# Kernel tuning notes

Measured on AMD Instinct MI355X. Metric: run time of the kernel, lower is better.

Reference implementation:

```python
import jax, jax.numpy as jnp
import numpy as np

WORD = 30000
NGRAM = 50000
F = WORD + NGRAM
B, L, K = 32, 64, 6
D, H, FFD, NL = 256, 8, 512, 2
EPS = 1e-5


def setup_inputs() -> dict:
    key = jax.random.key(0)
    ks = jax.random.split(key, 16)
    s = 0.02
    return {
        "word_idx": jax.random.randint(ks[0], (B, L), 0, WORD),
        "ngram_idx": jax.random.randint(ks[1], (B, L, K), 0, NGRAM),
        "fc1_w": jax.random.normal(ks[2], (FFD, F), jnp.float32) * s,
        "fc1_b": jax.random.normal(ks[3], (FFD,), jnp.float32) * s,
        "fc2_w": jax.random.normal(ks[4], (D, FFD), jnp.float32) * s,
        "fc2_b": jax.random.normal(ks[5], (D,), jnp.float32) * s,
        "qkv_w": jax.random.normal(ks[6], (NL, 3 * D, D), jnp.float32) * s,
        "qkv_b": jax.random.normal(ks[7], (NL, 3 * D), jnp.float32) * s,
        "out_w": jax.random.normal(ks[8], (NL, D, D), jnp.float32) * s,
        "out_b": jax.random.normal(ks[9], (NL, D), jnp.float32) * s,
        "ln1_g": jnp.ones((NL, D), jnp.float32),
        "ln1_b": jnp.zeros((NL, D), jnp.float32),
        "ff1_w": jax.random.normal(ks[10], (NL, 4 * D, D), jnp.float32) * s,
        "ff1_b": jax.random.normal(ks[11], (NL, 4 * D), jnp.float32) * s,
        "ff2_w": jax.random.normal(ks[12], (NL, D, 4 * D), jnp.float32) * s,
        "ff2_b": jax.random.normal(ks[13], (NL, D), jnp.float32) * s,
        "ln2_g": jnp.ones((NL, D), jnp.float32),
        "ln2_b": jnp.zeros((NL, D), jnp.float32),
    }


def _layer_norm(x, g, b):
    m = jnp.mean(x, axis=-1, keepdims=True)
    v = jnp.var(x, axis=-1, keepdims=True)
    return (x - m) * jax.lax.rsqrt(v + EPS) * g + b


def _sparse_vecs(word_idx, ngram_idx):
    # vectorized replacement of the per-token scatter loop: multi-hot [B,L,F]
    b, l = word_idx.shape
    bi = jnp.arange(b)[:, None]
    li = jnp.arange(l)[None, :]
    sv = jnp.zeros((b, l, F), jnp.float32)
    sv = sv.at[bi, li, word_idx].set(1.0)
    sv = sv.at[bi[:, :, None], li[:, :, None], WORD + ngram_idx].set(1.0)
    return sv


def reference(word_idx, ngram_idx, fc1_w, fc1_b, fc2_w, fc2_b, qkv_w, qkv_b,
              out_w, out_b, ln1_g, ln1_b, ff1_w, ff1_b, ff2_w, ff2_b,
              ln2_g, ln2_b):
    sv = _sparse_vecs(word_idx, ngram_idx)
    x = jax.nn.relu(sv @ fc1_w.T + fc1_b)          # [B,L,FFD]
    x = x @ fc2_w.T + fc2_b                        # [B,L,D]
    b, l, d = x.shape
    hd = d // H
    scale = 1.0 / np.sqrt(hd).astype(np.float32)
    for i in range(NL):  # post-norm TransformerEncoderLayer, eval mode (no dropout)
        qkv = x @ qkv_w[i].T + qkv_b[i]
        q, k, v = jnp.split(qkv, 3, axis=-1)
        q = q.reshape(b, l, H, hd).transpose(0, 2, 1, 3)
        k = k.reshape(b, l, H, hd).transpose(0, 2, 1, 3)
        v = v.reshape(b, l, H, hd).transpose(0, 2, 1, 3)
        attn = jax.nn.softmax(jnp.einsum('bhqd,bhkd->bhqk', q, k) * scale, axis=-1)
        o = jnp.einsum('bhqk,bhkd->bhqd', attn, v).transpose(0, 2, 1, 3).reshape(b, l, d)
        o = o @ out_w[i].T + out_b[i]
        x = _layer_norm(x + o, ln1_g[i], ln1_b[i])
        f = jax.nn.relu(x @ ff1_w[i].T + ff1_b[i]) @ ff2_w[i].T + ff2_b[i]
        x = _layer_norm(x + f, ln2_g[i], ln2_b[i])
    return x
```

## Files before the change

kernel.cpp:

```cpp
#include <hip/hip_runtime.h>
#include <hip/hip_bf16.h>
#include <math.h>

#define WORDC 30000
#define F_TOT 80000
#define NTOK  2048
#define DMODEL 256
#define FFDIM 512
#define NHEAD 8
#define HDIM  32
#define SEQL  64

typedef __attribute__((ext_vector_type(8))) short bf16x8;
typedef __attribute__((ext_vector_type(8))) unsigned short u16x8;
typedef __attribute__((ext_vector_type(4))) float f32x4;

__device__ __forceinline__ unsigned short f32_to_bf16_rne(float x) {
    unsigned int u = __float_as_uint(x);
    unsigned int r = (u + 0x7FFFu + ((u >> 16) & 1u)) >> 16;
    return (unsigned short)r;
}

__device__ __forceinline__ u16x8 cvt8(float4 a, float4 b) {
    u16x8 v;
    v[0] = f32_to_bf16_rne(a.x); v[1] = f32_to_bf16_rne(a.y);
    v[2] = f32_to_bf16_rne(a.z); v[3] = f32_to_bf16_rne(a.w);
    v[4] = f32_to_bf16_rne(b.x); v[5] = f32_to_bf16_rne(b.y);
    v[6] = f32_to_bf16_rne(b.z); v[7] = f32_to_bf16_rne(b.w);
    return v;
}

__global__ __launch_bounds__(256) void mark_feats_par(
    const int* __restrict__ word_idx,
    const int* __restrict__ ngram_idx,
    unsigned int* __restrict__ bm)
{
    int i = blockIdx.x * 256 + threadIdx.x;
    int f;
    if (i < NTOK)                f = word_idx[i];
    else if (i < NTOK * 7)       f = WORDC + ngram_idx[i - NTOK];
    else                         return;
    atomicOr(&bm[f >> 5], 1u << (f & 31));
}

__global__ __launch_bounds__(256) void transpose_cvt(
    const float* __restrict__ fc1_w,
    unsigned short* __restrict__ fc1T,
    const unsigned int* __restrict__ bm,
    const float* __restrict__ s0, const float* __restrict__ s1,
    const float* __restrict__ s2, const float* __restrict__ s3,
    unsigned short* __restrict__ d0, unsigned short* __restrict__ d1,
    unsigned short* __restrict__ d2, unsigned short* __restrict__ d3)
{
    __shared__ float tile[320][17];
    const int bid = blockIdx.x;
    const int tid = threadIdx.x;

    if (bid < 8000) {
        const int f0 = (bid % 250) * 320;
        const int j0 = (bid / 250) * 16;

        #pragma unroll
        for (int it = 0; it < 5; ++it) {
            int idx = it * 256 + tid;
            int jr  = idx / 80;
            int c4  = idx - jr * 80;
            float4 v = *(const float4*)&fc1_w[(long)(j0 + jr) * F_TOT + f0 + c4 * 4];
            tile[c4 * 4 + 0][jr] = v.x;
            tile[c4 * 4 + 1][jr] = v.y;
            tile[c4 * 4 + 2][jr] = v.z;
            tile[c4 * 4 + 3][jr] = v.w;
        }
        __syncthreads();

        for (int f = tid; f < 320; f += 256) {
            int fg = f0 + f;
            if ((bm[fg >> 5] >> (fg & 31)) & 1u) {
                u16x8 lo, hi;
                #pragma unroll
                for (int j = 0; j < 8; ++j) {
                    lo[j] = f32_to_bf16_rne(tile[f][j]);
                    hi[j] = f32_to_bf16_rne(tile[f][j + 8]);
                }
                *(u16x8*)&fc1T[(long)fg * FFDIM + j0]     = lo;
                *(u16x8*)&fc1T[(long)fg * FFDIM + j0 + 8] = hi;
            }
        }
    } else {
        int s = bid - 8000;
        int ten = s / 48, b48 = s % 48;
        const float* src; unsigned short* dst; int n4;
        switch (ten) {
            case 0:  src = s0; dst = d0; n4 = 2 * 768 * 256 / 4;  break;
            case 1:  src = s1; dst = d1; n4 = 2 * 256 * 256 / 4;  break;
            case 2:  src = s2; dst = d2; n4 = 2 * 1024 * 256 / 4; break;
            default: src = s3; dst = d3; n4 = 2 * 256 * 1024 / 4; break;
        }
        for (int i = b48 * 256 + tid; i < n4; i += 48 * 256) {
            float4 v = ((const float4*)src)[i];
            ushort4 o;
            o.x = f32_to_bf16_rne(v.x);
            o.y = f32_to_bf16_rne(v.y);
            o.z = f32_to_bf16_rne(v.z);
            o.w = f32_to_bf16_rne(v.w);
            ((ushort4*)dst)[i] = o;
        }
    }
}

__global__ __launch_bounds__(256) void embed_gather(
    const int* __restrict__ word_idx,
    const int* __restrict__ ngram_idx,
    const unsigned short* __restrict__ fc1_wT,
    const float* __restrict__ fc1_b,
    const float* __restrict__ fc2_w,
    const float* __restrict__ fc2_b,
    float* __restrict__ x)
{
    __shared__ int   feats[8][8];
    __shared__ float wmsk[8][8];
    __shared__ float x1[8][FFDIM];

    const int t0  = blockIdx.x * 8;
    const int tid = threadIdx.x;

    if (tid < 8) {
        int t = t0 + tid;
        feats[tid][0] = word_idx[t];
        wmsk[tid][0]  = 1.f;
        #pragma unroll
        for (int k = 0; k < 6; ++k) {
            int f = WORDC + ngram_idx[t * 6 + k];
            bool dup = false;
            for (int s = 1; s <= k; ++s)
                if (feats[tid][s] == f) dup = true;
            feats[tid][1 + k] = f;
            wmsk[tid][1 + k]  = dup ? 0.f : 1.f;
        }
    }
// ... 2 lines not shown
    const float2 bb = *(const float2*)&fc1_b[tid * 2];
    #pragma unroll
    for (int tt = 0; tt < 8; ++tt) {
        float a0 = bb.x, a1 = bb.y;
        #pragma unroll
        for (int s = 0; s < 7; ++s) {
            unsigned int wrd = *(const unsigned int*)
                &fc1_wT[(long)feats[tt][s] * FFDIM + tid * 2];
            float m = wmsk[tt][s];
            a0 += m * __uint_as_float((wrd & 0xFFFFu) << 16);
            a1 += m * __uint_as_float(wrd & 0xFFFF0000u);
        }
        x1[tt][tid * 2 + 0] = fmaxf(a0, 0.f);
        x1[tt][tid * 2 + 1] = fmaxf(a1, 0.f);
    }
    __syncthreads();

    const int d = tid;
    float acc[8];
    float cb = fc2_b[d];
    #pragma unroll
    for (int tt = 0; tt < 8; ++tt) acc[tt] = cb;
    const float* wrow = fc2_w + d * FFDIM;
    for (int k = 0; k < FFDIM; ++k) {
        float wv = wrow[k];
        #pragma unroll
        for (int tt = 0; tt < 8; ++tt) acc[tt] += wv * x1[tt][k];
    }
    #pragma unroll
    for (int tt = 0; tt < 8; ++tt)
        x[(t0 + tt) * DMODEL + d] = acc[tt];
}

__global__ __launch_bounds__(512) void fused_qkv_attn(
    const float* __restrict__ x,
    const unsigned short* __restrict__ Wq,
    const float* __restrict__ bq,
    float* __restrict__ o)
{
    __shared__ unsigned short sA[64 * 264];
    __shared__ unsigned short sWp[8][48 * 72];
    __shared__ unsigned short sQ[64 * 40];
    __shared__ unsigned short sK[64 * 40];
    __shared__ unsigned short sVt[32 * 72];
    __shared__ unsigned short sP[64 * 72];
    __shared__ float sfmx[2][64];
    __shared__ float sfsm[2][64];

    const int b = blockIdx.x >> 3;
    const int h = blockIdx.x & 7;
    const int tid  = threadIdx.x;
    const int lane = tid & 63;
    const int w    = tid >> 6;
    const int rg   = w & 3;
    const int ch   = w >> 2;
    const int fr   = lane & 15;
    const int ksub = lane >> 4;
    const int row0 = b * SEQL;

    #pragma unroll
    for (int j = 0; j < 4; ++j) {
        int c = j * 512 + tid;
        int row = c >> 5, c8 = c & 31;
        const float* ap = &x[(long)(row0 + row) * DMODEL + c8 * 8];
        float4 a0 = *(const float4*)ap;
        float4 a1 = *(const float4*)(ap + 4);
        *(u16x8*)&sA[row * 264 + c8 * 8] = cvt8(a0, a1);
    }

    int lr6[6], grow6[6];
    const int wcc = (lane & 7) * 8;
    #pragma unroll
    for (int j = 0; j < 6; ++j) {
        int lr = j * 8 + (lane >> 3);
        lr6[j] = lr;
        int c = ch * 48 + lr;
        grow6[j] = (c >> 5) * 256 + h * HDIM + (c & 31);
    }
    u16x8 wc[6], wn[6];
    #pragma unroll
    for (int j = 0; j < 6; ++j)
        wc[j] = *(const u16x8*)&Wq[(long)grow6[j] * DMODEL + wcc];

    __syncthreads();

    f32x4 acc[3] = {};
    for (int t = 0; t < 4; ++t) {
        #pragma unroll
        for (int j = 0; j < 6; ++j)
            *(u16x8*)&sWp[w][lr6[j] * 72 + wcc] = wc[j];
        if (t < 3) {
            int k0 = (t + 1) * 64;
            #pragma unroll
            for (int j = 0; j < 6; ++j)
                wn[j] = *(const u16x8*)&Wq[(long)grow6[j] * DMODEL + k0 + wcc];
        }
        #pragma unroll
        for (int kk = 0; kk < 2; ++kk) {
            bf16x8 af = *(bf16x8*)&sA[(rg * 16 + fr) * 264 + t * 64 + kk * 32 + ksub * 8];
            #pragma unroll
            for (int ni = 0; ni < 3; ++ni) {
                bf16x8 bf = *(bf16x8*)&sWp[w][(ni * 16 + fr) * 72 + kk * 32 + ksub * 8];
                acc[ni] = __builtin_amdgcn_mfma_f32_16x16x32_bf16(af, bf, acc[ni], 0, 0, 0);
            }
        }
        if (t < 3) {
            #pragma unroll
            for (int j = 0; j < 6; ++j) wc[j] = wn[j];
        }
    }

    const float scale = 0.17677669529663687f;
    #pragma unroll
    for (int ni = 0; ni < 3; ++ni) {
        int c = ch * 48 + ni * 16 + fr;
        int part = c >> 5, pc = c & 31;
        float bv = bq[part * 256 + h * HDIM + pc];
        #pragma unroll
        for (int r = 0; r < 4; ++r) {
            int row = rg * 16 + ksub * 4 + r;
            float v = acc[ni][r] + bv;
            if (part == 0)      sQ[row * 40 + pc] = f32_to_bf16_rne(v * scale);
            else if (part == 1) sK[row * 40 + pc] = f32_to_bf16_rne(v);
            else                sVt[pc * 72 + row] = f32_to_bf16_rne(v);
        }
    }
    __syncthreads();

    f32x4 s4[2];
    {
        bf16x8 afq = *(bf16x8*)&sQ[(rg * 16 + fr) * 40 + ksub * 8];
        #pragma unroll
        for (int ni = 0; ni < 2; ++ni) {
            bf16x8 bfk = *(bf16x8*)&sK[(ch * 32 + ni * 16 + fr) * 40 + ksub * 8];
            f32x4 z = {};
            s4[ni] = __builtin_amdgcn_mfma_f32_16x16x32_bf16(afq, bfk, z, 0, 0, 0);
        }
    }

    #pragma unroll
    for (int r = 0; r < 4; ++r) {
// ... 12 lines not shown
        float m = fmaxf(sfmx[0][row], sfmx[1][row]);
        float p0 = __expf(s4[0][r] - m);
        float p1 = __expf(s4[1][r] - m);
        sP[row * 72 + ch * 32 + fr]      = f32_to_bf16_rne(p0);
        sP[row * 72 + ch * 32 + 16 + fr] = f32_to_bf16_rne(p1);
        float s = p0 + p1;
        s += __shfl_xor(s, 1);
        s += __shfl_xor(s, 2);
        s += __shfl_xor(s, 4);
        s += __shfl_xor(s, 8);
        if (fr == 0) sfsm[ch][row] = s;
    }
    __syncthreads();
    #pragma unroll
    for (int r = 0; r < 4; ++r) {
        int row = rg * 16 + ksub * 4 + r;
        minv[r] = 1.f / (sfsm[0][row] + sfsm[1][row]);
    }

    f32x4 o4 = {};
    #pragma unroll
    for (int kc = 0; kc < 2; ++kc) {
        bf16x8 afp = *(bf16x8*)&sP[(rg * 16 + fr) * 72 + kc * 32 + ksub * 8];
        bf16x8 bfv = *(bf16x8*)&sVt[(ch * 16 + fr) * 72 + kc * 32 + ksub * 8];
        o4 = __builtin_amdgcn_mfma_f32_16x16x32_bf16(afp, bfv, o4, 0, 0, 0);
    }
    #pragma unroll
    for (int r = 0; r < 4; ++r) {
        int row = row0 + rg * 16 + ksub * 4 + r;
        o[(long)row * DMODEL + h * HDIM + ch * 16 + fr] = o4[r] * minv[r];
    }
}

__global__ __launch_bounds__(512) void outln_ffn(
    const float* __restrict__ attn_raw,
    const unsigned short* __restrict__ Wo,
    const float* __restrict__ bo,
    const float* __restrict__ g1, const float* __restrict__ b1t,
    const unsigned short* __restrict__ W1,
    const float* __restrict__ b1,
    const unsigned short* __restrict__ W2,
    const float* __restrict__ b2,
    const float* __restrict__ g2, const float* __restrict__ b2t,
    float* __restrict__ x)
{
    __shared__ unsigned short sA[16 * 264];
    __shared__ float xnf[8 * 264];
    __shared__ unsigned short x1s[16 * 1032];
    __shared__ unsigned short sWp[8][32 * 72];
    __shared__ float redS[8][8];
    __shared__ float redQ[8][8];

    const int tid  = threadIdx.x;
    const int lane = tid & 63;
    const int w    = tid >> 6;
    const int fr   = lane & 15;
    const int ksub = lane >> 4;
    const int m0   = blockIdx.x * 8;

    const int lrb = lane >> 3;
    const int wcc = (lane & 7) * 8;

    {
        int row = tid >> 5, c8 = tid & 31;
        if (tid < 256) {
            const float* ap = &attn_raw[(long)(m0 + row) * DMODEL + c8 * 8];
            float4 a0 = *(const float4*)ap;
            float4 a1 = *(const float4*)(ap + 4);
            *(u16x8*)&sA[row * 264 + c8 * 8] = cvt8(a0, a1);
        } else {
            u16x8 z = {};
            *(u16x8*)&sA[row * 264 + c8 * 8] = z;
        }
    }

    u16x8 wc[4], wn[4];
    #pragma unroll
    for (int j = 0; j < 4; ++j)
        wc[j] = *(const u16x8*)&Wo[(long)(w * 32 + j * 8 + lrb) * DMODEL + wcc];

    __syncthreads();

    f32x4 acc[2] = {};
    #pragma unroll
    for (int t = 0; t < 4; ++t) {
        #pragma unroll
        for (int j = 0; j < 4; ++j)
            *(u16x8*)&sWp[w][(j * 8 + lrb) * 72 + wcc] = wc[j];
        if (t < 3) {
            int k0 = (t + 1) * 64;
            #pragma unroll
            for (int j = 0; j < 4; ++j)
                wn[j] = *(const u16x8*)&Wo[(long)(w * 32 + j * 8 + lrb) * DMODEL + k0 + wcc];
        }
        #pragma unroll
        for (int kk = 0; kk < 2; ++kk) {
            bf16x8 af = *(bf16x8*)&sA[fr * 264 + t * 64 + kk * 32 + ksub * 8];
            #pragma unroll
            for (int ni = 0; ni < 2; ++ni) {
                bf16x8 bf = *(bf16x8*)&sWp[w][(ni * 16 + fr) * 72 + kk * 32 + ksub * 8];
                acc[ni] = __builtin_amdgcn_mfma_f32_16x16x32_bf16(af, bf, acc[ni], 0, 0, 0);
            }
        }
        if (t < 3) {
            #pragma unroll
            for (int j = 0; j < 4; ++j) wc[j] = wn[j];
        }
    }

    float vres[2][4];
    #pragma unroll
    for (int ni = 0; ni < 2; ++ni) {
        int col = w * 32 + ni * 16 + fr;
        float bv = bo[col];
        #pragma unroll
        for (int r = 0; r < 4; ++r) {
            int rl = ksub * 4 + r;
            vres[ni][r] = (rl < 8)
                ? acc[ni][r] + bv + x[(long)(m0 + rl) * DMODEL + col]
                : 0.f;
        }
    }

    #pragma unroll
    for (int r = 0; r < 4; ++r) {
        float s  = vres[0][r] + vres[1][r];
        float qq = vres[0][r] * vres[0][r] + vres[1][r] * vres[1][r];
        #pragma unroll
        for (int mask = 1; mask < 16; mask <<= 1) {
            s  += __shfl_xor(s, mask);
            qq += __shfl_xor(qq, mask);
        }
        if (fr == 0 && ksub < 2) {
            redS[w][ksub * 4 + r] = s;
            redQ[w][ksub * 4 + r] = qq;
        }
    }
    #pragma unroll
    for (int j = 0; j < 4; ++j)
        wc[j] = *(const u16x8*)&W1[(long)(w * 32 + j * 8 + lrb) * DMODEL + wcc];

    __syncthreads();

    #pragma unroll
    for (int r = 0; r < 4; ++r) {
        int rl = ksub * 4 + r;
        if (rl < 8) {
            float sum = 0.f, sumq = 0.f;
            #pragma unroll
            for (int ww = 0; ww < 8; ++ww) {
                sum  += redS[ww][rl];
                sumq += redQ[ww][rl];
            }
            float mean = sum * (1.f / 256.f);
            float var  = sumq * (1.f / 256.f) - mean * mean;
            float rstd = rsqrtf(var + 1e-5f);
            #pragma unroll
            for (int ni = 0; ni < 2; ++ni) {
                int col = w * 32 + ni * 16 + fr;
                float v = (vres[ni][r] - mean) * rstd * g1[col] + b1t[col];
                xnf[rl * 264 + col] = v;
                sA[rl * 264 + col] = f32_to_bf16_rne(v);
            }
        }
    }
    __syncthreads();

    f32x4 acc2[2] = {};
    for (int t = 0; t < 32; ++t) {
        #pragma unroll
        for (int j = 0; j < 4; ++j)
            *(u16x8*)&sWp[w][(j * 8 + lrb) * 72 + wcc] = wc[j];
        if (t < 31) {
            int tn = t + 1;
            if (tn < 16) {
                int nc = tn >> 2, kq = tn & 3;
                #pragma unroll
                for (int j = 0; j < 4; ++j)
                    wn[j] = *(const u16x8*)&W1[(long)(nc * 256 + w * 32 + j * 8 + lrb) * DMODEL
                                               + kq * 64 + wcc];
            } else {
                int t2 = tn - 16;
                #pragma unroll
                for (int j = 0; j < 4; ++j)
                    wn[j] = *(const u16x8*)&W2[(long)(w * 32 + j * 8 + lrb) * 1024
                                               + t2 * 64 + wcc];
            }
        }
        #pragma unroll
        for (int kk = 0; kk < 2; ++kk) {
            bf16x8 af;
            if (t < 16)
                af = *(bf16x8*)&sA[fr * 264 + (t & 3) * 64 + kk * 32 + ksub * 8];
            else
                af = *(bf16x8*)&x1s[fr * 1032 + (t - 16) * 64 + kk * 32 + ksub * 8];
            #pragma unroll
            for (int ni = 0; ni < 2; ++ni) {
                bf16x8 bf = *(bf16x8*)&sWp[w][(ni * 16 + fr) * 72 + kk * 32 + ksub * 8];
                acc2[ni] = __builtin_amdgcn_mfma_f32_16x16x32_bf16(af, bf, acc2[ni], 0, 0, 0);
            }
        }
        if (t < 16 && (t & 3) == 3) {
            int nc = t >> 2;
            #pragma unroll
            for (int ni = 0; ni < 2; ++ni) {
                int col = nc * 256 + w * 32 + ni * 16 + fr;
                float bv = b1[col];
                #pragma unroll
                for (int r = 0; r < 4; ++r) {
                    int rl = ksub * 4 + r;
                    x1s[rl * 1032 + col] = (rl < 8)
                        ? f32_to_bf16_rne(fmaxf(acc2[ni][r] + bv, 0.f))
                        : (unsigned short)0;
                }
                acc2[ni] = (f32x4){};
            }
        }
        if (t == 15) __syncthreads();
        if (t < 31) {
            #pragma unroll
            for (int j = 0; j < 4; ++j) wc[j] = wn[j];
        }
    }

    float vres2[2][4];
    #pragma unroll
    for (int ni = 0; ni < 2; ++ni) {
        int col = w * 32 + ni * 16 + fr;
        float bv = b2[col];
        #pragma unroll
        for (int r = 0; r < 4; ++r) {
            int rl = ksub * 4 + r;
            vres2[ni][r] = (rl < 8)
                ? acc2[ni][r] + bv + xnf[rl * 264 + col]
                : 0.f;
        }
    }

    #pragma unroll
    for (int r = 0; r < 4; ++r) {
        float s  = vres2[0][r] + vres2[1][r];
        float qq = vres2[0][r] * vres2[0][r] + vres2[1][r] * vres2[1][r];
        #pragma unroll
        for (int mask = 1; mask < 16; mask <<= 1) {
            s  += __shfl_xor(s, mask);
            qq += __shfl_xor(qq, mask);
        }
        if (fr == 0 && ksub < 2) {
            redS[w][ksub * 4 + r] = s;
            redQ[w][ksub * 4 + r] = qq;
        }
    }
    __syncthreads();

    #pragma unroll
    for (int r = 0; r < 4; ++r) {
        int rl = ksub * 4 + r;
        if (rl < 8) {
            float sum = 0.f, sumq = 0.f;
            #pragma unroll
            for (int ww = 0; ww < 8; ++ww) {
                sum  += redS[ww][rl];
                sumq += redQ[ww][rl];
            }
            float mean = sum * (1.f / 256.f);
            float var  = sumq * (1.f / 256.f) - mean * mean;
            float rstd = rsqrtf(var + 1e-5f);
            #pragma unroll
            for (int ni = 0; ni < 2; ++ni) {
                int col = w * 32 + ni * 16 + fr;
                x[(long)(m0 + rl) * DMODEL + col] =
                    (vres2[ni][r] - mean) * rstd * g2[col] + b2t[col];
            }
        }
    }
}

__global__ __launch_bounds__(256) void embed_kernel(
    const int* __restrict__ word_idx,
    const int* __restrict__ ngram_idx,
    const float* __restrict__ fc1_w,
    const float* __restrict__ fc1_b,
    const float* __restrict__ fc2_w,
    const float* __restrict__ fc2_b,
    float* __restrict__ x)
{
    __shared__ int   feats[8][8];
    __shared__ int   nf[8];
    __shared__ float x1[8][FFDIM];

    const int t0  = blockIdx.x * 8;
    const int tid = threadIdx.x;

    if (tid < 8) {
        int t = t0 + tid;
        int cnt = 0;
        feats[tid][cnt++] = word_idx[t];
        for (int k = 0; k < 6; ++k) {
            int f = WORDC + ngram_idx[t * 6 + k];
            bool dup = false;
            for (int s = 1; s < cnt; ++s)
                if (feats[tid][s] == f) dup = true;
            if (!dup) feats[tid][cnt++] = f;
        }
        nf[tid] = cnt;
    }
    __syncthreads();

// ... 141 lines not shown
        float s = 0.f;
        #pragma unroll
        for (int d = 0; d < HDIM; ++d) s += qreg[d] * Kt[jj][d];
        sc[i] = s;
        mx = fmaxf(mx, s);
    }
    mx = fmaxf(mx, __shfl_xor(mx, 1));
    mx = fmaxf(mx, __shfl_xor(mx, 2));

    float sum = 0.f;
    #pragma unroll
    for (int i = 0; i < 16; ++i) {
        float e = __expf(sc[i] - mx);
        S[q][p * 16 + i] = e;
        sum += e;
    }
    sum += __shfl_xor(sum, 1);
    sum += __shfl_xor(sum, 2);
    const float inv = 1.f / sum;
    __syncthreads();

    float acc[8] = {};
    for (int jj = 0; jj < SEQL; ++jj) {
        float pv = S[q][jj];
        #pragma unroll
        for (int d = 0; d < 8; ++d) acc[d] += pv * Vt[jj][p * 8 + d];
    }
    float* orow = o + (long)(b * SEQL + q) * DMODEL + h * HDIM + p * 8;
    float4 o0, o1;
    o0.x = acc[0] * inv; o0.y = acc[1] * inv; o0.z = acc[2] * inv; o0.w = acc[3] * inv;
    o1.x = acc[4] * inv; o1.y = acc[5] * inv; o1.z = acc[6] * inv; o1.w = acc[7] * inv;
    *(float4*)orow = o0;
    *(float4*)(orow + 4) = o1;
}

__global__ __launch_bounds__(256) void add_ln_kernel(
    const float* __restrict__ xin,
    const float* __restrict__ f,
    const float* __restrict__ g,
    const float* __restrict__ bta,
    float* __restrict__ xout)
{
    const int w = threadIdx.x >> 6;
    const int lane = threadIdx.x & 63;
    const int t = blockIdx.x * 4 + w;

    float4 xv = *(const float4*)&xin[(long)t * DMODEL + lane * 4];
    float4 fv = *(const float4*)&f[(long)t * DMODEL + lane * 4];
    float v0 = xv.x + fv.x, v1 = xv.y + fv.y, v2 = xv.z + fv.z, v3 = xv.w + fv.w;

    float s  = v0 + v1 + v2 + v3;
    float sq = v0 * v0 + v1 * v1 + v2 * v2 + v3 * v3;
    #pragma unroll
    for (int off = 1; off < 64; off <<= 1) {
        s  += __shfl_xor(s, off);
        sq += __shfl_xor(sq, off);
    }
    float mean = s * (1.f / 256.f);
    float var  = sq * (1.f / 256.f) - mean * mean;
    float rs   = rsqrtf(var + 1e-5f);

    float4 gv = *(const float4*)&g[lane * 4];
    float4 bv = *(const float4*)&bta[lane * 4];
    float4 o;
    o.x = (v0 - mean) * rs * gv.x + bv.x;
    o.y = (v1 - mean) * rs * gv.y + bv.y;
    o.z = (v2 - mean) * rs * gv.z + bv.z;
    o.w = (v3 - mean) * rs * gv.w + bv.w;
    *(float4*)&xout[(long)t * DMODEL + lane * 4] = o;
}

extern "C" void kernel_launch(void* const* d_in, const int* in_sizes, int n_in,
                              void* d_out, int out_size, void* d_ws, size_t ws_size,
                              hipStream_t stream) {
    const int*   word_idx  = (const int*)d_in[0];
    const int*   ngram_idx = (const int*)d_in[1];
    const float* fc1_w = (const float*)d_in[2];
    const float* fc1_b = (const float*)d_in[3];
    const float* fc2_w = (const float*)d_in[4];
    const float* fc2_b = (const float*)d_in[5];
    const float* qkv_w = (const float*)d_in[6];
    const float* qkv_b = (const float*)d_in[7];
    const float* out_w = (const float*)d_in[8];
    const float* out_b = (const float*)d_in[9];
    const float* ln1_g = (const float*)d_in[10];
    const float* ln1_b = (const float*)d_in[11];
    const float* ff1_w = (const float*)d_in[12];
    const float* ff1_b = (const float*)d_in[13];
    const float* ff2_w = (const float*)d_in[14];
    const float* ff2_b = (const float*)d_in[15];
    const float* ln2_g = (const float*)d_in[16];
    const float* ln2_b = (const float*)d_in[17];

    float* x = (float*)d_out;

    const size_t BM_OFF   = 0;
    const size_t FC1T_OFF = 10240;
    const size_t FC1T_BYTES = (size_t)F_TOT * FFDIM * 2;
    const size_t QKVT_OFF = FC1T_OFF + FC1T_BYTES;
    const size_t QKVT_BYTES = (size_t)2 * 768 * 256 * 2;
    const size_t OUTT_OFF = QKVT_OFF + QKVT_BYTES;
    const size_t OUTT_BYTES = (size_t)2 * 256 * 256 * 2;
    const size_t FF1T_OFF = OUTT_OFF + OUTT_BYTES;
    const size_t FF1T_BYTES = (size_t)2 * 1024 * 256 * 2;
    const size_t FF2T_OFF = FF1T_OFF + FF1T_BYTES;
    const size_t FF2T_BYTES = (size_t)2 * 256 * 1024 * 2;
    const size_t ATTN_OFF = FF2T_OFF + FF2T_BYTES;
    const size_t ATTN_BYTES = (size_t)NTOK * DMODEL * 4;
    const size_t FAST_BYTES = ATTN_OFF + ATTN_BYTES;

    if (ws_size >= FAST_BYTES) {
        unsigned int*   bm   = (unsigned int*)((char*)d_ws + BM_OFF);
        unsigned short* fc1T = (unsigned short*)((char*)d_ws + FC1T_OFF);
        unsigned short* qkvT = (unsigned short*)((char*)d_ws + QKVT_OFF);
        unsigned short* outT = (unsigned short*)((char*)d_ws + OUTT_OFF);
        unsigned short* ff1T = (unsigned short*)((char*)d_ws + FF1T_OFF);
        unsigned short* ff2T = (unsigned short*)((char*)d_ws + FF2T_OFF);
        float* attn_raw = (float*)((char*)d_ws + ATTN_OFF);

        hipMemsetAsync((void*)bm, 0, 10240, stream);
        mark_feats_par<<<56, 256, 0, stream>>>(word_idx, ngram_idx, bm);
        transpose_cvt<<<8192, 256, 0, stream>>>(
            fc1_w, fc1T, bm, qkv_w, out_w, ff1_w, ff2_w, qkvT, outT, ff1T, ff2T);
        embed_gather<<<NTOK / 8, 256, 0, stream>>>(word_idx, ngram_idx, fc1T,
                                                   fc1_b, fc2_w, fc2_b, x);

        for (int i = 0; i < 2; ++i) {
            fused_qkv_attn<<<32 * NHEAD, 512, 0, stream>>>(
                x, qkvT + (long)i * 768 * 256, qkv_b + i * 768, attn_raw);

            outln_ffn<<<NTOK / 8, 512, 0, stream>>>(
                attn_raw, outT + (long)i * 256 * 256, out_b + i * 256,
                ln1_g + i * 256, ln1_b + i * 256,
                ff1T + (long)i * 1024 * 256, ff1_b + i * 1024,
                ff2T + (long)i * 256 * 1024, ff2_b + i * 256,
                ln2_g + i * 256, ln2_b + i * 256, x);
        }
    } else {
        float* wsf      = (float*)d_ws;
        float* qkvbuf   = wsf;
        float* attn_raw = qkvbuf + 2048 * 768;
        float* obuf     = attn_raw + 2048 * 256;
        float* ffbuf    = obuf + 2048 * 256;

        embed_kernel<<<NTOK / 8, 256, 0, stream>>>(word_idx, ngram_idx, fc1_w,
                                                   fc1_b, fc2_w, fc2_b, x);
        for (int i = 0; i < 2; ++i) {
            gemm_bias<false><<<dim3(768 / 64, NTOK / 64), 256, 0, stream>>>(
                x, qkv_w + (long)i * 768 * 256, qkv_b + i * 768, qkvbuf,
                NTOK, 768, 256);
            attn_kernel<<<32 * NHEAD, 256, 0, stream>>>(qkvbuf, attn_raw);
            gemm_bias<false><<<dim3(256 / 64, NTOK / 64), 256, 0, stream>>>(
                attn_raw, out_w + (long)i * 256 * 256, out_b + i * 256, obuf,
                NTOK, 256, 256);
            add_ln_kernel<<<NTOK / 4, 256, 0, stream>>>(x, obuf, ln1_g + i * 256,
                                                        ln1_b + i * 256, x);
            gemm_bias<true><<<dim3(1024 / 64, NTOK / 64), 256, 0, stream>>>(
                x, ff1_w + (long)i * 1024 * 256, ff1_b + i * 1024, ffbuf,
                NTOK, 1024, 256);
            gemm_bias<false><<<dim3(256 / 64, NTOK / 64), 256, 0, stream>>>(
                ffbuf, ff2_w + (long)i * 256 * 1024, ff2_b + i * 256, obuf,
                NTOK, 256, 1024);
            add_ln_kernel<<<NTOK / 4, 256, 0, stream>>>(x, obuf, ln2_g + i * 256,
                                                        ln2_b + i * 256, x);
        }
    }
}
```

Baseline: 133.7 us.

## Split fused out-proj/FFN kernel into separate tiled bf16 GEMMs plus add-LN

After: 148.3 us. +10.9%, slower.

```diff
diff --git a/kernel.cpp b/kernel.cpp
--- a/kernel.cpp
+++ b/kernel.cpp
@@ -222,19 +222,33 @@
     #pragma unroll
     for (int j = 0; j < 6; ++j)
         wc[j] = *(const u16x8*)&Wq[(long)grow6[j] * DMODEL + wcc];
+    #pragma unroll
+    for (int j = 0; j < 6; ++j)
+        wn[j] = *(const u16x8*)&Wq[(long)grow6[j] * DMODEL + 64 + wcc];
 
     __syncthreads();
 
     f32x4 acc[3] = {};
+    #pragma unroll
     for (int t = 0; t < 4; ++t) {
-        #pragma unroll
-        for (int j = 0; j < 6; ++j)
-            *(u16x8*)&sWp[w][lr6[j] * 72 + wcc] = wc[j];
-        if (t < 3) {
-            int k0 = (t + 1) * 64;
+        if ((t & 1) == 0) {
             #pragma unroll
             for (int j = 0; j < 6; ++j)
-                wn[j] = *(const u16x8*)&Wq[(long)grow6[j] * DMODEL + k0 + wcc];
+                *(u16x8*)&sWp[w][lr6[j] * 72 + wcc] = wc[j];
+            if (t + 2 < 4) {
+                #pragma unroll
+                for (int j = 0; j < 6; ++j)
+                    wc[j] = *(const u16x8*)&Wq[(long)grow6[j] * DMODEL + (t + 2) * 64 + wcc];
+            }
+        } else {
+            #pragma unroll
+            for (int j = 0; j < 6; ++j)
+                *(u16x8*)&sWp[w][lr6[j] * 72 + wcc] = wn[j];
+            if (t + 2 < 4) {
+                #pragma unroll
+                for (int j = 0; j < 6; ++j)
+                    wn[j] = *(const u16x8*)&Wq[(long)grow6[j] * DMODEL + (t + 2) * 64 + wcc];
+            }
         }
         #pragma unroll
         for (int kk = 0; kk < 2; ++kk) {
@@ -244,10 +258,6 @@
                 bf16x8 bf = *(bf16x8*)&sWp[w][(ni * 16 + fr) * 72 + kk * 32 + ksub * 8];
                 acc[ni] = __builtin_amdgcn_mfma_f32_16x16x32_bf16(af, bf, acc[ni], 0, 0, 0);
             }
-        }
-        if (t < 3) {
-            #pragma unroll
-            for (int j = 0; j < 6; ++j) wc[j] = wn[j];
         }
     }
 
@@ -326,21 +336,16 @@
     }
 }
 
-__global__ __launch_bounds__(512) void outln_ffn(
+__global__ __launch_bounds__(512) void outln(
     const float* __restrict__ attn_raw,
     const unsigned short* __restrict__ Wo,
     const float* __restrict__ bo,
     const float* __restrict__ g1, const float* __restrict__ b1t,
-    const unsigned short* __restrict__ W1,
-    const float* __restrict__ b1,
-    const unsigned short* __restrict__ W2,
-    const float* __restrict__ b2,
-    const float* __restrict__ g2, const float* __restrict__ b2t,
-    float* __restrict__ x)
+    const float* __restrict__ x,
+    unsigned short* __restrict__ xnb,
+    float* __restrict__ xnf)
 {
     __shared__ unsigned short sA[16 * 264];
-    __shared__ float xnf[8 * 264];
-    __shared__ unsigned short x1s[16 * 1032];
     __shared__ unsigned short sWp[8][32 * 72];
     __shared__ float redS[8][8];
     __shared__ float redQ[8][8];
@@ -430,10 +435,6 @@
             redQ[w][ksub * 4 + r] = qq;
         }
     }
-    #pragma unroll
-    for (int j = 0; j < 4; ++j)
-        wc[j] = *(const u16x8*)&W1[(long)(w * 32 + j * 8 + lrb) * DMODEL + wcc];
-
     __syncthreads();
 
     #pragma unroll
@@ -453,121 +454,116 @@
             for (int ni = 0; ni < 2; ++ni) {
                 int col = w * 32 + ni * 16 + fr;
                 float v = (vres[ni][r] - mean) * rstd * g1[col] + b1t[col];
-                xnf[rl * 264 + col] = v;
-                sA[rl * 264 + col] = f32_to_bf16_rne(v);
+                long idx = (long)(m0 + rl) * DMODEL + col;
+                xnf[idx] = v;
+                xnb[idx] = f32_to_bf16_rne(v);
             }
         }
     }
-    __syncthreads();
-
-    f32x4 acc2[2] = {};
-    for (int t = 0; t < 32; ++t) {
-        #pragma unroll
-        for (int j = 0; j < 4; ++j)
-            *(u16x8*)&sWp[w][(j * 8 + lrb) * 72 + wcc] = wc[j];
-        if (t < 31) {
-            int tn = t + 1;
-            if (tn < 16) {
-                int nc = tn >> 2, kq = tn & 3;
-                #pragma unroll
-                for (int j = 0; j < 4; ++j)
-                    wn[j] = *(const u16x8*)&W1[(long)(nc * 256 + w * 32 + j * 8 + lrb) * DMODEL
-                                               + kq * 64 + wcc];
-            } else {
-                int t2 = tn - 16;
-                #pragma unroll
-                for (int j = 0; j < 4; ++j)
-                    wn[j] = *(const u16x8*)&W2[(long)(w * 32 + j * 8 + lrb) * 1024
-                                               + t2 * 64 + wcc];
+}
+
+template<bool RELU, bool OUT16>
+__global__ __launch_bounds__(256) void gemm_bf16(
+    const unsigned short* __restrict__ A,
+    const unsigned short* __restrict__ Wb,
+    const float* __restrict__ bias,
+    void* __restrict__ Cout,
+    int M, int N, int K)
+{
+    __shared__ unsigned short sA[64 * 40];
+    __shared__ unsigned short sW[64 * 40];
+
+    const int tid  = threadIdx.x;
+    const int lane = tid & 63;
+    const int w    = tid >> 6;
+    const int wr   = w >> 1;
+    const int wc   = w & 1;
+    const int m0   = blockIdx.y * 64;
+    const int n0   = blockIdx.x * 64;
+
+    const int srow = tid >> 2;
+    const int ssub = tid & 3;
+
+    const int fr   = lane & 15;
+    const int ksub = lane >> 4;
+
+    f32x4 acc[2][2] = {};
+
+    for (int k0 = 0; k0 < K; k0 += 32) {
+        u16x8 av = *(const u16x8*)&A[(long)(m0 + srow) * K + k0 + ssub * 8];
+        u16x8 wv = *(const u16x8*)&Wb[(long)(n0 + srow) * K + k0 + ssub * 8];
+
+        __syncthreads();
+        *(u16x8*)&sA[srow * 40 + ssub * 8] = av;
+        *(u16x8*)&sW[srow * 40 + ssub * 8] = wv;
+        __syncthreads();
+
+        #pragma unroll
+        for (int mi = 0; mi < 2; ++mi) {
+            bf16x8 af = *(bf16x8*)&sA[(wr * 32 + mi * 16 + fr) * 40 + ksub * 8];
+            #pragma unroll
+            for (int ni = 0; ni < 2; ++ni) {
+                bf16x8 bf = *(bf16x8*)&sW[(wc * 32 + ni * 16 + fr) * 40 + ksub * 8];
+                acc[mi][ni] = __builtin_amdgcn_mfma_f32_16x16x32_bf16(
+                    af, bf, acc[mi][ni], 0, 0, 0);
             }
         }
-        #pragma unroll
-        for (int kk = 0; kk < 2; ++kk) {
-            bf16x8 af;
-            if (t < 16)
-                af = *(bf16x8*)&sA[fr * 264 + (t & 3) * 64 + kk * 32 + ksub * 8];
-            else
-                af = *(bf16x8*)&x1s[fr * 1032 + (t - 16) * 64 + kk * 32 + ksub * 8];
-            #pragma unroll
-            for (int ni = 0; ni < 2; ++ni) {
-                bf16x8 bf = *(bf16x8*)&sWp[w][(ni * 16 + fr) * 72 + kk * 32 + ksub * 8];
-                acc2[ni] = __builtin_amdgcn_mfma_f32_16x16x32_bf16(af, bf, acc2[ni], 0, 0, 0);
+    }
+
+    #pragma unroll
+    for (int mi = 0; mi < 2; ++mi) {
+        #pragma unroll
+        for (int ni = 0; ni < 2; ++ni) {
+            int col = n0 + wc * 32 + ni * 16 + fr;
+            float bv = bias[col];
+            #pragma unroll
+            for (int r = 0; r < 4; ++r) {
+                int row = m0 + wr * 32 + mi * 16 + ksub * 4 + r;
+                float v = acc[mi][ni][r] + bv;
+                if (RELU) v = fmaxf(v, 0.f);
+                if (OUT16)
+                    ((unsigned short*)Cout)[(long)row * N + col] = f32_to_bf16_rne(v);
+                else
+                    ((float*)Cout)[(long)row * N + col] = v;
             }
         }
-        if (t < 16 && (t & 3) == 3) {
-            int nc = t >> 2;
-            #pragma unroll
-            for (int ni = 0; ni < 2; ++ni) {
-                int col = nc * 256 + w * 32 + ni * 16 + fr;
-                float bv = b1[col];
-                #pragma unroll
-                for (int r = 0; r < 4; ++r) {
-                    int rl = ksub * 4 + r;
-                    x1s[rl * 1032 + col] = (rl < 8)
-                        ? f32_to_bf16_rne(fmaxf(acc2[ni][r] + bv, 0.f))
-                        : (unsigned short)0;
-                }
-                acc2[ni] = (f32x4){};
-            }
-        }
-        if (t == 15) __syncthreads();
-        if (t < 31) {
-            #pragma unroll
-            for (int j = 0; j < 4; ++j) wc[j] = wn[j];
-        }
-    }
-
-    float vres2[2][4];
-    #pragma unroll
-    for (int ni = 0; ni < 2; ++ni) {
-        int col = w * 32 + ni * 16 + fr;
-        float bv = b2[col];
-        #pragma unroll
-        for (int r = 0; r < 4; ++r) {
-            int rl = ksub * 4 + r;
-            vres2[ni][r] = (rl < 8)
-                ? acc2[ni][r] + bv + xnf[rl * 264 + col]
-                : 0.f;
-        }
-    }
-
-    #pragma unroll
-    for (int r = 0; r < 4; ++r) {
-        float s  = vres2[0][r] + vres2[1][r];
-        float qq = vres2[0][r] * vres2[0][r] + vres2[1][r] * vres2[1][r];
-        #pragma unroll
-        for (int mask = 1; mask < 16; mask <<= 1) {
-            s  += __shfl_xor(s, mask);
-            qq += __shfl_xor(qq, mask);
-        }
-        if (fr == 0 && ksub < 2) {
-            redS[w][ksub * 4 + r] = s;
-            redQ[w][ksub * 4 + r] = qq;
-        }
-    }
-    __syncthreads();
-
-    #pragma unroll
-    for (int r = 0; r < 4; ++r) {
-        int rl = ksub * 4 + r;
-        if (rl < 8) {
-            float sum = 0.f, sumq = 0.f;
-            #pragma unroll
-            for (int ww = 0; ww < 8; ++ww) {
-                sum  += redS[ww][rl];
-                sumq += redQ[ww][rl];
-            }
-            float mean = sum * (1.f / 256.f);
-            float var  = sumq * (1.f / 256.f) - mean * mean;
-            float rstd = rsqrtf(var + 1e-5f);
-            #pragma unroll
-            for (int ni = 0; ni < 2; ++ni) {
-                int col = w * 32 + ni * 16 + fr;
-                x[(long)(m0 + rl) * DMODEL + col] =
-                    (vres2[ni][r] - mean) * rstd * g2[col] + b2t[col];
-            }
-        }
-    }
+    }
+}
+
+__global__ __launch_bounds__(256) void add_ln_kernel(
+    const float* __restrict__ xin,
+    const float* __restrict__ f,
+    const float* __restrict__ g,
+    const float* __restrict__ bta,
+    float* __restrict__ xout)
+{
+    const int w = threadIdx.x >> 6;
+    const int lane = threadIdx.x & 63;
+    const int t = blockIdx.x * 4 + w;
+
+    float4 xv = *(const float4*)&xin[(long)t * DMODEL + lane * 4];
+    float4 fv = *(const float4*)&f[(long)t * DMODEL + lane * 4];
+    float v0 = xv.x + fv.x, v1 = xv.y + fv.y, v2 = xv.z + fv.z, v3 = xv.w + fv.w;
+
+    float s  = v0 + v1 + v2 + v3;
+    float sq = v0 * v0 + v1 * v1 + v2 * v2 + v3 * v3;
+    #pragma unroll
+    for (int off = 1; off < 64; off <<= 1) {
+        s  += __shfl_xor(s, off);
+        sq += __shfl_xor(sq, off);
+    }
+    float mean = s * (1.f / 256.f);
+    float var  = sq * (1.f / 256.f) - mean * mean;
+    float rs   = rsqrtf(var + 1e-5f);
+
+    float4 gv = *(const float4*)&g[lane * 4];
+    float4 bv = *(const float4*)&bta[lane * 4];
+    float4 o;
+    o.x = (v0 - mean) * rs * gv.x + bv.x;
+    o.y = (v1 - mean) * rs * gv.y + bv.y;
+    o.z = (v2 - mean) * rs * gv.z + bv.z;
+    o.w = (v3 - mean) * rs * gv.w + bv.w;
+    *(float4*)&xout[(long)t * DMODEL + lane * 4] = o;
 }
 
 __global__ __launch_bounds__(256) void embed_kernel(
@@ -775,42 +771,6 @@
     o1.x = acc[4] * inv; o1.y = acc[5] * inv; o1.z = acc[6] * inv; o1.w = acc[7] * inv;
     *(float4*)orow = o0;
     *(float4*)(orow + 4) = o1;
-}
-
-__global__ __launch_bounds__(256) void add_ln_kernel(
-    const float* __restrict__ xin,
-    const float* __restrict__ f,
-    const float* __restrict__ g,
-    const float* __restrict__ bta,
-    float* __restrict__ xout)
-{
-    const int w = threadIdx.x >> 6;
-    const int lane = threadIdx.x & 63;
-    const int t = blockIdx.x * 4 + w;
-
-    float4 xv = *(const float4*)&xin[(long)t * DMODEL + lane * 4];
-    float4 fv = *(const float4*)&f[(long)t * DMODEL + lane * 4];
-    float v0 = xv.x + fv.x, v1 = xv.y + fv.y, v2 = xv.z + fv.z, v3 = xv.w + fv.w;
-
-    float s  = v0 + v1 + v2 + v3;
-    float sq = v0 * v0 + v1 * v1 + v2 * v2 + v3 * v3;
-    #pragma unroll
-    for (int off = 1; off < 64; off <<= 1) {
-        s  += __shfl_xor(s, off);
-        sq += __shfl_xor(sq, off);
-    }
-    float mean = s * (1.f / 256.f);
-    float var  = sq * (1.f / 256.f) - mean * mean;
-    float rs   = rsqrtf(var + 1e-5f);
-
-    float4 gv = *(const float4*)&g[lane * 4];
-    float4 bv = *(const float4*)&bta[lane * 4];
-    float4 o;
-    o.x = (v0 - mean) * rs * gv.x + bv.x;
-    o.y = (v1 - mean) * rs * gv.y + bv.y;
-    o.z = (v2 - mean) * rs * gv.z + bv.z;
-    o.w = (v3 - mean) * rs * gv.w + bv.w;
-    *(float4*)&xout[(long)t * DMODEL + lane * 4] = o;
 }
 
 extern "C" void kernel_launch(void* const* d_in, const int* in_sizes, int n_in,
@@ -850,7 +810,15 @@
     const size_t FF2T_BYTES = (size_t)2 * 256 * 1024 * 2;
     const size_t ATTN_OFF = FF2T_OFF + FF2T_BYTES;
     const size_t ATTN_BYTES = (size_t)NTOK * DMODEL * 4;
-    const size_t FAST_BYTES = ATTN_OFF + ATTN_BYTES;
+    const size_t XNB_OFF  = ATTN_OFF + ATTN_BYTES;
+    const size_t XNB_BYTES = (size_t)NTOK * DMODEL * 2;
+    const size_t XNF_OFF  = XNB_OFF + XNB_BYTES;
+    const size_t XNF_BYTES = (size_t)NTOK * DMODEL * 4;
+    const size_t FFB_OFF  = XNF_OFF + XNF_BYTES;
+    const size_t FFB_BYTES = (size_t)NTOK * 1024 * 2;
+    const size_t OBUF_OFF = FFB_OFF + FFB_BYTES;
+    const size_t OBUF_BYTES = (size_t)NTOK * DMODEL * 4;
+    const size_t FAST_BYTES = OBUF_OFF + OBUF_BYTES;
 
     if (ws_size >= FAST_BYTES) {
         unsigned int*   bm   = (unsigned int*)((char*)d_ws + BM_OFF);
@@ -860,6 +828,10 @@
         unsigned short* ff1T = (unsigned short*)((char*)d_ws + FF1T_OFF);
         unsigned short* ff2T = (unsigned short*)((char*)d_ws + FF2T_OFF);
         float* attn_raw = (float*)((char*)d_ws + ATTN_OFF);
+        unsigned short* xnb = (unsigned short*)((char*)d_ws + XNB_OFF);
+        float* xnf = (float*)((char*)d_ws + XNF_OFF);
+        unsigned short* ffb = (unsigned short*)((char*)d_ws + FFB_OFF);
+        float* obuf = (float*)((char*)d_ws + OBUF_OFF);
 
         hipMemsetAsync((void*)bm, 0, 10240, stream);
         mark_feats_par<<<56, 256, 0, stream>>>(word_idx, ngram_idx, bm);
@@ -872,12 +844,20 @@
             fused_qkv_attn<<<32 * NHEAD, 512, 0, stream>>>(
                 x, qkvT + (long)i * 768 * 256, qkv_b + i * 768, attn_raw);
 
-            outln_ffn<<<NTOK / 8, 512, 0, stream>>>(
+            outln<<<NTOK / 8, 512, 0, stream>>>(
                 attn_raw, outT + (long)i * 256 * 256, out_b + i * 256,
-                ln1_g + i * 256, ln1_b + i * 256,
-                ff1T + (long)i * 1024 * 256, ff1_b + i * 1024,
-                ff2T + (long)i * 256 * 1024, ff2_b + i * 256,
-                ln2_g + i * 256, ln2_b + i * 256, x);
+                ln1_g + i * 256, ln1_b + i * 256, x, xnb, xnf);
+
+            gemm_bf16<true, true><<<dim3(1024 / 64, NTOK / 64), 256, 0, stream>>>(
+                xnb, ff1T + (long)i * 1024 * 256, ff1_b + i * 1024, ffb,
+                NTOK, 1024, 256);
+
+            gemm_bf16<false, false><<<dim3(256 / 64, NTOK / 64), 256, 0, stream>>>(
+                ffb, ff2T + (long)i * 256 * 1024, ff2_b + i * 256, obuf,
+                NTOK, 256, 1024);
+
+            add_ln_kernel<<<NTOK / 4, 256, 0, stream>>>(
+                xnf, obuf, ln2_g + i * 256, ln2_b + i * 256, x);
         }
     } else {
         float* wsf      = (float*)d_ws;
```

## Pre-pack transformer weights into MFMA fragment layout and load fragments directly

Applied to the files above, without the earlier changes.

Result: faster. 125.4 us (-6.2%).

```diff
diff --git a/kernel.cpp b/kernel.cpp
--- a/kernel.cpp
+++ b/kernel.cpp
@@ -28,6 +28,11 @@
     v[4] = f32_to_bf16_rne(b.x); v[5] = f32_to_bf16_rne(b.y);
     v[6] = f32_to_bf16_rne(b.z); v[7] = f32_to_bf16_rne(b.w);
     return v;
+}
+
+__device__ __forceinline__ bf16x8 ldfrag(const unsigned short* F, int ntile,
+                                          int KT, int ktile, int lane) {
+    return *(const bf16x8*)&F[(((long)(ntile * KT + ktile) * 64 + lane) << 3)];
 }
 
 __global__ __launch_bounds__(256) void mark_feats_par(
@@ -87,24 +92,24 @@
             }
         }
     } else {
-        int s = bid - 8000;
-        int ten = s / 48, b48 = s % 48;
-        const float* src; unsigned short* dst; int n4;
-        switch (ten) {
-            case 0:  src = s0; dst = d0; n4 = 2 * 768 * 256 / 4;  break;
-            case 1:  src = s1; dst = d1; n4 = 2 * 256 * 256 / 4;  break;
-            case 2:  src = s2; dst = d2; n4 = 2 * 1024 * 256 / 4; break;
-            default: src = s3; dst = d3; n4 = 2 * 256 * 1024 / 4; break;
-        }
-        for (int i = b48 * 256 + tid; i < n4; i += 48 * 256) {
-            float4 v = ((const float4*)src)[i];
-            ushort4 o;
-            o.x = f32_to_bf16_rne(v.x);
-            o.y = f32_to_bf16_rne(v.y);
-            o.z = f32_to_bf16_rne(v.z);
-            o.w = f32_to_bf16_rne(v.w);
-            ((ushort4*)dst)[i] = o;
-        }
+        long fid = (long)(bid - 8000) * 256 + tid;
+        const float* src; unsigned short* dst; int K; long base;
+        if (fid < 49152)        { src = s0; dst = d0; K = 256;  base = fid; }
+        else if (fid < 65536)   { src = s1; dst = d1; K = 256;  base = fid - 49152; }
+        else if (fid < 131072)  { src = s2; dst = d2; K = 256;  base = fid - 65536; }
+        else                    { src = s3; dst = d3; K = 1024; base = fid - 131072; }
+        int lane = (int)(base & 63);
+        long t   = base >> 6;
+        int KT   = K >> 5;
+        int ntile = (int)(t / KT);
+        int ktile = (int)(t - (long)ntile * KT);
+        int row = ntile * 16 + (lane & 15);
+        int k   = ktile * 32 + (lane >> 4) * 8;
+        const float* sp = src + (long)row * K + k;
+        u16x8 v;
+        #pragma unroll
+        for (int j = 0; j < 8; ++j) v[j] = f32_to_bf16_rne(sp[j]);
+        *(u16x8*)&dst[base << 3] = v;
     }
 }
 
@@ -173,14 +178,13 @@
         x[(t0 + tt) * DMODEL + d] = acc[tt];
 }
 
-__global__ __launch_bounds__(512) void fused_qkv_attn(
+__global__ __launch_bounds__(512, 4) void fused_qkv_attn(
     const float* __restrict__ x,
-    const unsigned short* __restrict__ Wq,
+    const unsigned short* __restrict__ WqF,
     const float* __restrict__ bq,
     float* __restrict__ o)
 {
     __shared__ unsigned short sA[64 * 264];
-    __shared__ unsigned short sWp[8][48 * 72];
     __shared__ unsigned short sQ[64 * 40];
     __shared__ unsigned short sK[64 * 40];
     __shared__ unsigned short sVt[32 * 72];
@@ -199,6 +203,14 @@
     const int ksub = lane >> 4;
     const int row0 = b * SEQL;
 
+    int nt[3];
+    #pragma unroll
+    for (int ni = 0; ni < 3; ++ni) {
+        int c = ch * 48 + ni * 16;
+        int part = c >> 5, pcb = c & 31;
+        nt[ni] = (part * 256 + h * HDIM + pcb) >> 4;
+    }
+
     #pragma unroll
     for (int j = 0; j < 4; ++j) {
         int c = j * 512 + tid;
@@ -209,45 +221,37 @@
         *(u16x8*)&sA[row * 264 + c8 * 8] = cvt8(a0, a1);
     }
 
-    int lr6[6], grow6[6];
-    const int wcc = (lane & 7) * 8;
-    #pragma unroll
-    for (int j = 0; j < 6; ++j) {
-        int lr = j * 8 + (lane >> 3);
-        lr6[j] = lr;
-        int c = ch * 48 + lr;
-        grow6[j] = (c >> 5) * 256 + h * HDIM + (c & 31);
-    }
-    u16x8 wc[6], wn[6];
-    #pragma unroll
-    for (int j = 0; j < 6; ++j)
-        wc[j] = *(const u16x8*)&Wq[(long)grow6[j] * DMODEL + wcc];
+    bf16x8 wf[2][2][3];
+    #pragma unroll
+    for (int kk = 0; kk < 2; ++kk)
+        #pragma unroll
+        for (int ni = 0; ni < 3; ++ni)
+            wf[0][kk][ni] = ldfrag(WqF, nt[ni], 8, kk, lane);
+    #pragma unroll
+    for (int kk = 0; kk < 2; ++kk)
+        #pragma unroll
+        for (int ni = 0; ni < 3; ++ni)
+            wf[1][kk][ni] = ldfrag(WqF, nt[ni], 8, 2 + kk, lane);
 
     __syncthreads();
 
     f32x4 acc[3] = {};
+    #pragma unroll
     for (int t = 0; t < 4; ++t) {
-        #pragma unroll
-        for (int j = 0; j < 6; ++j)
-            *(u16x8*)&sWp[w][lr6[j] * 72 + wcc] = wc[j];
-        if (t < 3) {
-            int k0 = (t + 1) * 64;
-            #pragma unroll
-            for (int j = 0; j < 6; ++j)
-                wn[j] = *(const u16x8*)&Wq[(long)grow6[j] * DMODEL + k0 + wcc];
-        }
+        const int cur = t & 1;
         #pragma unroll
         for (int kk = 0; kk < 2; ++kk) {
             bf16x8 af = *(bf16x8*)&sA[(rg * 16 + fr) * 264 + t * 64 + kk * 32 + ksub * 8];
             #pragma unroll
-            for (int ni = 0; ni < 3; ++ni) {
-                bf16x8 bf = *(bf16x8*)&sWp[w][(ni * 16 + fr) * 72 + kk * 32 + ksub * 8];
-                acc[ni] = __builtin_amdgcn_mfma_f32_16x16x32_bf16(af, bf, acc[ni], 0, 0, 0);
-            }
-        }
-        if (t < 3) {
-            #pragma unroll
-            for (int j = 0; j < 6; ++j) wc[j] = wn[j];
+            for (int ni = 0; ni < 3; ++ni)
+                acc[ni] = __builtin_amdgcn_mfma_f32_16x16x32_bf16(af, wf[cur][kk][ni], acc[ni], 0, 0, 0);
+        }
+        if (t + 2 < 4) {
+            #pragma unroll
+            for (int kk = 0; kk < 2; ++kk)
+                #pragma unroll
+                for (int ni = 0; ni < 3; ++ni)
+                    wf[cur][kk][ni] = ldfrag(WqF, nt[ni], 8, (t + 2) * 2 + kk, lane);
         }
     }
 
@@ -326,14 +330,14 @@
     }
 }
 
-__global__ __launch_bounds__(512) void outln_ffn(
+__global__ __launch_bounds__(512, 4) void outln_ffn(
     const float* __restrict__ attn_raw,
-    const unsigned short* __restrict__ Wo,
+    const unsigned short* __restrict__ WoF,
     const float* __restrict__ bo,
     const float* __restrict__ g1, const float* __restrict__ b1t,
-    const unsigned short* __restrict__ W1,
+    const unsigned short* __restrict__ W1F,
     const float* __restrict__ b1,
-    const unsigned short* __restrict__ W2,
+    const unsigned short* __restrict__ W2F,
     const float* __restrict__ b2,
     const float* __restrict__ g2, const float* __restrict__ b2t,
     float* __restrict__ x)
@@ -341,7 +345,6 @@
     __shared__ unsigned short sA[16 * 264];
     __shared__ float xnf[8 * 264];
     __shared__ unsigned short x1s[16 * 1032];
-    __shared__ unsigned short sWp[8][32 * 72];
     __shared__ float redS[8][8];
     __shared__ float redQ[8][8];
 
@@ -351,9 +354,6 @@
     const int fr   = lane & 15;
     const int ksub = lane >> 4;
     const int m0   = blockIdx.x * 8;
-
-    const int lrb = lane >> 3;
-    const int wcc = (lane & 7) * 8;
 
     {
         int row = tid >> 5, c8 = tid & 31;
@@ -368,37 +368,37 @@
         }
     }
 
-    u16x8 wc[4], wn[4];
-    #pragma unroll
-    for (int j = 0; j < 4; ++j)
-        wc[j] = *(const u16x8*)&Wo[(long)(w * 32 + j * 8 + lrb) * DMODEL + wcc];
+    bf16x8 wf[2][2][2];
+    #pragma unroll
+    for (int kk = 0; kk < 2; ++kk)
+        #pragma unroll
+        for (int ni = 0; ni < 2; ++ni)
+            wf[0][kk][ni] = ldfrag(WoF, w * 2 + ni, 8, kk, lane);
+    #pragma unroll
+    for (int kk = 0; kk < 2; ++kk)
+        #pragma unroll
+        for (int ni = 0; ni < 2; ++ni)
+            wf[1][kk][ni] = ldfrag(WoF, w * 2 + ni, 8, 2 + kk, lane);
 
     __syncthreads();
 
     f32x4 acc[2] = {};
     #pragma unroll
     for (int t = 0; t < 4; ++t) {
-        #pragma unroll
-        for (int j = 0; j < 4; ++j)
-            *(u16x8*)&sWp[w][(j * 8 + lrb) * 72 + wcc] = wc[j];
-        if (t < 3) {
-            int k0 = (t + 1) * 64;
-            #pragma unroll
-            for (int j = 0; j < 4; ++j)
-                wn[j] = *(const u16x8*)&Wo[(long)(w * 32 + j * 8 + lrb) * DMODEL + k0 + wcc];
-        }
+        const int cur = t & 1;
         #pragma unroll
         for (int kk = 0; kk < 2; ++kk) {
             bf16x8 af = *(bf16x8*)&sA[fr * 264 + t * 64 + kk * 32 + ksub * 8];
             #pragma unroll
-            for (int ni = 0; ni < 2; ++ni) {
-                bf16x8 bf = *(bf16x8*)&sWp[w][(ni * 16 + fr) * 72 + kk * 32 + ksub * 8];
-                acc[ni] = __builtin_amdgcn_mfma_f32_16x16x32_bf16(af, bf, acc[ni], 0, 0, 0);
-            }
-        }
-        if (t < 3) {
-            #pragma unroll
-            for (int j = 0; j < 4; ++j) wc[j] = wn[j];
+            for (int ni = 0; ni < 2; ++ni)
+                acc[ni] = __builtin_amdgcn_mfma_f32_16x16x32_bf16(af, wf[cur][kk][ni], acc[ni], 0, 0, 0);
+        }
+        if (t + 2 < 4) {
+            #pragma unroll
+            for (int kk = 0; kk < 2; ++kk)
+                #pragma unroll
+                for (int ni = 0; ni < 2; ++ni)
+                    wf[cur][kk][ni] = ldfrag(WoF, w * 2 + ni, 8, (t + 2) * 2 + kk, lane);
         }
     }
 
@@ -416,6 +416,15 @@
         }
     }
 
+    bf16x8 wc[2][2], wn[2][2], wn2[2][2];
+    #pragma unroll
+    for (int kk = 0; kk < 2; ++kk)
+        #pragma unroll
+        for (int ni = 0; ni < 2; ++ni) {
+            wc[kk][ni] = ldfrag(W1F, w * 2 + ni, 8, kk, lane);
+            wn[kk][ni] = ldfrag(W1F, w * 2 + ni, 8, 2 + kk, lane);
+        }
+
     #pragma unroll
     for (int r = 0; r < 4; ++r) {
         float s  = vres[0][r] + vres[1][r];
@@ -430,10 +439,6 @@
             redQ[w][ksub * 4 + r] = qq;
         }
     }
-    #pragma unroll
-    for (int j = 0; j < 4; ++j)
-        wc[j] = *(const u16x8*)&W1[(long)(w * 32 + j * 8 + lrb) * DMODEL + wcc];
-
     __syncthreads();
 
     #pragma unroll
@@ -462,23 +467,22 @@
 
     f32x4 acc2[2] = {};
     for (int t = 0; t < 32; ++t) {
-        #pragma unroll
-        for (int j = 0; j < 4; ++j)
-            *(u16x8*)&sWp[w][(j * 8 + lrb) * 72 + wcc] = wc[j];
-        if (t < 31) {
-            int tn = t + 1;
+        if (t < 30) {
+            int tn = t + 2;
             if (tn < 16) {
                 int nc = tn >> 2, kq = tn & 3;
                 #pragma unroll
-                for (int j = 0; j < 4; ++j)
-                    wn[j] = *(const u16x8*)&W1[(long)(nc * 256 + w * 32 + j * 8 + lrb) * DMODEL
-                                               + kq * 64 + wcc];
+                for (int kk = 0; kk < 2; ++kk)
+                    #pragma unroll
+                    for (int ni = 0; ni < 2; ++ni)
+                        wn2[kk][ni] = ldfrag(W1F, nc * 16 + w * 2 + ni, 8, kq * 2 + kk, lane);
             } else {
                 int t2 = tn - 16;
                 #pragma unroll
-                for (int j = 0; j < 4; ++j)
-                    wn[j] = *(const u16x8*)&W2[(long)(w * 32 + j * 8 + lrb) * 1024
-                                               + t2 * 64 + wcc];
+                for (int kk = 0; kk < 2; ++kk)
+                    #pragma unroll
+                    for (int ni = 0; ni < 2; ++ni)
+                        wn2[kk][ni] = ldfrag(W2F, w * 2 + ni, 32, t2 * 2 + kk, lane);
             }
         }
         #pragma unroll
@@ -489,10 +493,8 @@
             else
                 af = *(bf16x8*)&x1s[fr * 1032 + (t - 16) * 64 + kk * 32 + ksub * 8];
             #pragma unroll
-            for (int ni = 0; ni < 2; ++ni) {
-                bf16x8 bf = *(bf16x8*)&sWp[w][(ni * 16 + fr) * 72 + kk * 32 + ksub * 8];
-                acc2[ni] = __builtin_amdgcn_mfma_f32_16x16x32_bf16(af, bf, acc2[ni], 0, 0, 0);
-            }
+            for (int ni = 0; ni < 2; ++ni)
+                acc2[ni] = __builtin_amdgcn_mfma_f32_16x16x32_bf16(af, wc[kk][ni], acc2[ni], 0, 0, 0);
         }
         if (t < 16 && (t & 3) == 3) {
             int nc = t >> 2;
@@ -511,10 +513,13 @@
             }
         }
         if (t == 15) __syncthreads();
-        if (t < 31) {
-            #pragma unroll
-            for (int j = 0; j < 4; ++j) wc[j] = wn[j];
-        }
+        #pragma unroll
+        for (int kk = 0; kk < 2; ++kk)
+            #pragma unroll
+            for (int ni = 0; ni < 2; ++ni) {
+                wc[kk][ni] = wn[kk][ni];
+                wn[kk][ni] = wn2[kk][ni];
+            }
     }
 
     float vres2[2][4];
@@ -855,28 +860,28 @@
     if (ws_size >= FAST_BYTES) {
         unsigned int*   bm   = (unsigned int*)((char*)d_ws + BM_OFF);
         unsigned short* fc1T = (unsigned short*)((char*)d_ws + FC1T_OFF);
-        unsigned short* qkvT = (unsigned short*)((char*)d_ws + QKVT_OFF);
-        unsigned short* outT = (unsigned short*)((char*)d_ws + OUTT_OFF);
-        unsigned short* ff1T = (unsigned short*)((char*)d_ws + FF1T_OFF);
-        unsigned short* ff2T = (unsigned short*)((char*)d_ws + FF2T_OFF);
+        unsigned short* qkvF = (unsigned short*)((char*)d_ws + QKVT_OFF);
+        unsigned short* outF = (unsigned short*)((char*)d_ws + OUTT_OFF);
+        unsigned short* ff1F = (unsigned short*)((char*)d_ws + FF1T_OFF);
+        unsigned short* ff2F = (unsigned short*)((char*)d_ws + FF2T_OFF);
         float* attn_raw = (float*)((char*)d_ws + ATTN_OFF);
 
         hipMemsetAsync((void*)bm, 0, 10240, stream);
         mark_feats_par<<<56, 256, 0, stream>>>(word_idx, ngram_idx, bm);
-        transpose_cvt<<<8192, 256, 0, stream>>>(
-            fc1_w, fc1T, bm, qkv_w, out_w, ff1_w, ff2_w, qkvT, outT, ff1T, ff2T);
+        transpose_cvt<<<8768, 256, 0, stream>>>(
+            fc1_w, fc1T, bm, qkv_w, out_w, ff1_w, ff2_w, qkvF, outF, ff1F, ff2F);
         embed_gather<<<NTOK / 8, 256, 0, stream>>>(word_idx, ngram_idx, fc1T,
                                                    fc1_b, fc2_w, fc2_b, x);
 
         for (int i = 0; i < 2; ++i) {
             fused_qkv_attn<<<32 * NHEAD, 512, 0, stream>>>(
-                x, qkvT + (long)i * 768 * 256, qkv_b + i * 768, attn_raw);
+                x, qkvF + (long)i * 768 * 256, qkv_b + i * 768, attn_raw);
 
             outln_ffn<<<NTOK / 8, 512, 0, stream>>>(
-                attn_raw, outT + (long)i * 256 * 256, out_b + i * 256,
+                attn_raw, outF + (long)i * 256 * 256, out_b + i * 256,
                 ln1_g + i * 256, ln1_b + i * 256,
-                ff1T + (long)i * 1024 * 256, ff1_b + i * 1024,
-                ff2T + (long)i * 256 * 1024, ff2_b + i * 256,
+                ff1F + (long)i * 1024 * 256, ff1_b + i * 1024,
+                ff2F + (long)i * 256 * 1024, ff2_b + i * 256,
                 ln2_g + i * 256, ln2_b + i * 256, x);
         }
     } else {
```
